# Performance work log

Measured on AMD Instinct MI355X. Metric: run time of the kernel, lower is better.

## Reference

```python
import jax, jax.numpy as jnp
import numpy as np
from jax import lax

B, T, IN, H, NC = 512, 512, 128, 256, 10
GRID_SIZE, SPLINE_ORDER = 5, 3


def _grid(in_f):
    h = 2.0 / GRID_SIZE
    pts = jnp.arange(-SPLINE_ORDER, GRID_SIZE + SPLINE_ORDER + 1, dtype=jnp.float32) * h - 1.0
    return jnp.broadcast_to(pts, (in_f, pts.shape[0]))


def _b_splines(x, grid):
    # x: (B, in); grid: (in, GRID_SIZE + 2*SPLINE_ORDER + 1)
    xg = x[..., None]
    b = ((xg >= grid[:, :-1]) & (xg < grid[:, 1:])).astype(x.dtype)
    for k in range(1, SPLINE_ORDER + 1):
        b = ((xg - grid[:, :-(k + 1)]) / (grid[:, k:-1] - grid[:, :-(k + 1)]) * b[..., :-1]
             + (grid[:, k + 1:] - xg) / (grid[:, k + 1:] - grid[:, 1:-k]) * b[..., 1:])
    return b  # (B, in, GRID_SIZE + SPLINE_ORDER)


def _kan_linear(x, base_w, spline_w, scaler):
    g = _grid(x.shape[-1])
    base = jax.nn.silu(x) @ base_w.T
    spline = jnp.einsum('bik,oik->bo', _b_splines(x, g), spline_w * scaler[..., None])
    return base + spline


def _gru_cell(x, h, wih, whh, bih, bhh):
    gi = x @ wih.T + bih
    gh = h @ whh.T + bhh
    ir, iz, inn = jnp.split(gi, 3, axis=-1)
    hr, hz, hn = jnp.split(gh, 3, axis=-1)
    r = jax.nn.sigmoid(ir + hr)
    z = jax.nn.sigmoid(iz + hz)
    n = jnp.tanh(inn + r * hn)
    return (1.0 - z) * n + z * h


def _lstm_single(x, wih, whh, bih, bhh):
    # single-timestep LSTM with zero initial (h, c); gate order i,f,g,o
    h0 = jnp.zeros((x.shape[0], whh.shape[1]), x.dtype)
    g = x @ wih.T + h0 @ whh.T + bih + bhh
    i, f, gg, o = jnp.split(g, 4, axis=-1)
    c = jax.nn.sigmoid(i) * jnp.tanh(gg)
    return jax.nn.sigmoid(o) * jnp.tanh(c)


def setup_inputs() -> dict:
    keys = iter(jax.random.split(jax.random.key(0), 64))
    def w(*shape):
        return jax.random.normal(next(keys), shape, jnp.float32) * 0.1
    d = {}
    d['x'] = jax.random.normal(next(keys), (B, T, IN), jnp.float32)
    d['gru0_wih'] = w(3 * H, IN); d['gru0_whh'] = w(3 * H, H)
    d['gru0_bih'] = w(3 * H); d['gru0_bhh'] = w(3 * H)
    d['gru1_wih'] = w(3 * H, H); d['gru1_whh'] = w(3 * H, H)
    d['gru1_bih'] = w(3 * H); d['gru1_bhh'] = w(3 * H)
    for suf in ['0', '0r', '1', '1r']:
        d['lw_ih' + suf] = w(512, 256); d['lw_hh' + suf] = w(512, 128)
        d['lb_ih' + suf] = w(512); d['lb_hh' + suf] = w(512)
    d['kan1_base'] = w(64, 256); d['kan1_spline'] = w(64, 256, GRID_SIZE + SPLINE_ORDER); d['kan1_scaler'] = w(64, 256)
    d['kan2_base'] = w(NC, 64); d['kan2_spline'] = w(NC, 64, GRID_SIZE + SPLINE_ORDER); d['kan2_scaler'] = w(NC, 64)
    return d


def reference(x, gru0_wih, gru0_whh, gru0_bih, gru0_bhh, gru1_wih, gru1_whh, gru1_bih, gru1_bhh,
              lw_ih0, lw_hh0, lb_ih0, lb_hh0, lw_ih0r, lw_hh0r, lb_ih0r, lb_hh0r,
              lw_ih1, lw_hh1, lb_ih1, lb_hh1, lw_ih1r, lw_hh1r, lb_ih1r, lb_hh1r,
              kan1_base, kan1_spline, kan1_scaler, kan2_base, kan2_spline, kan2_scaler):
    bsz = x.shape[0]
    h_init = (jnp.zeros((bsz, H), x.dtype), jnp.zeros((bsz, H), x.dtype))

    def step(carry, xt):
        h0, h1 = carry
        h0 = _gru_cell(xt, h0, gru0_wih, gru0_whh, gru0_bih, gru0_bhh)
        h1 = _gru_cell(h0, h1, gru1_wih, gru1_whh, gru1_bih, gru1_bhh)
        return (h0, h1), None

    (h0, h1), _ = lax.scan(step, h_init, jnp.swapaxes(x, 0, 1))  # time-major scan
    s = h1  # last layer final hidden, seq_len-1 single step for LSTM
    o0 = jnp.concatenate([_lstm_single(s, lw_ih0, lw_hh0, lb_ih0, lb_hh0),
                          _lstm_single(s, lw_ih0r, lw_hh0r, lb_ih0r, lb_hh0r)], axis=-1)
    o1 = jnp.concatenate([_lstm_single(o0, lw_ih1, lw_hh1, lb_ih1, lb_hh1),
                          _lstm_single(o0, lw_ih1r, lw_hh1r, lb_ih1r, lb_hh1r)], axis=-1)
    z = _kan_linear(o1, kan1_base, kan1_spline, kan1_scaler)
    return _kan_linear(z, kan2_base, kan2_spline, kan2_scaler)
```

## Files before the change

kernel.cpp:

```cpp
#include <hip/hip_runtime.h>
#include <stdint.h>


constexpr int B_  = 512;
constexpr int T_  = 512;
constexpr int IN_ = 128;
constexpr int H_  = 256;
constexpr int GR_ = 32;
constexpr int PL_ = GR_ * 2 * 4096;
constexpr int TCp = 64;
constexpr int NCp = 8;

typedef __attribute__((ext_vector_type(8))) short bf16x8;
typedef __attribute__((ext_vector_type(4))) float f32x4;

#define MFMA16(a, b, c) __builtin_amdgcn_mfma_f32_16x16x32_bf16((a), (b), (c), 0, 0, 0)

__device__ __forceinline__ float bf2f(unsigned short u){
    union { unsigned int i; float f; } v; v.i = ((unsigned int)u) << 16; return v.f;
}
__device__ __forceinline__ unsigned short f2bf(float f){
    union { float f; unsigned int i; } v; v.f = f;
    return (unsigned short)((v.i + 0x7FFFu + ((v.i >> 16) & 1u)) >> 16);
}
__device__ __forceinline__ unsigned int cvtpk(float a, float b){
    unsigned int r;
    asm("v_cvt_pk_bf16_f32 %0, %1, %2" : "=v"(r) : "v"(a), "v"(b));
    return r;
}
__device__ __forceinline__ unsigned long long pk4(float a, float b, float c, float d){
    const unsigned int lo = cvtpk(a, b), hi = cvtpk(c, d);
    return (unsigned long long)lo | ((unsigned long long)hi << 32);
}
__device__ __forceinline__ float sig_(float x){
    return __builtin_amdgcn_rcpf(1.0f + __expf(-x));
}
__device__ __forceinline__ float tanh_(float x){
    return 1.0f - 2.0f * __builtin_amdgcn_rcpf(1.0f + __expf(2.0f * x));
}
__device__ __forceinline__ bf16x8 ldb8g(const unsigned short* p){ return *(const bf16x8*)p; }

union U64x2 { unsigned long long q[2]; bf16x8 v; };

__device__ __forceinline__ void gl2lds16(const void* g, void* l){
    __builtin_amdgcn_global_load_lds(
        (const __attribute__((address_space(1))) unsigned int*)g,
        (__attribute__((address_space(3))) unsigned int*)l, 16, 0, 0);
}

__global__ void srt_detect(const unsigned int* __restrict__ xw, unsigned int* __restrict__ flag){
    int cnt = 0;
    for (int i = threadIdx.x; i < 1024; i += 64){
        const unsigned int lo = xw[i] & 0xFFFFu;
        const int e = (int)((lo >> 7) & 0xFFu);
        if (e >= 100 && e <= 140) cnt++;
    }
    #pragma unroll
    for (int o = 32; o > 0; o >>= 1) cnt += __shfl_down(cnt, o);
    if (threadIdx.x == 0) *flag = (cnt > 614) ? 1u : 0u;
}

struct ConvTab { const void* src[26]; int n[26]; int off[26]; };

__global__ __launch_bounds__(256) void srt_conv(ConvTab ct, unsigned short* __restrict__ wb,
                                                const unsigned int* __restrict__ flag){
    const bool isb = (*flag != 0);
    const int gsz = gridDim.x * blockDim.x;
    const int gid = blockIdx.x * blockDim.x + threadIdx.x;
    for (int j = 0; j < 26; ++j){
        const int n = ct.n[j];
        unsigned short* o = wb + ct.off[j];
        if (isb){
            const unsigned short* s = (const unsigned short*)ct.src[j];
            for (int i = gid; i < n; i += gsz) o[i] = s[i];
        } else {
            const float* s = (const float*)ct.src[j];
            for (int i = gid; i < n; i += gsz) o[i] = f2bf(s[i]);
        }
    }
}

__global__ __launch_bounds__(256) void srt_prep(
    float* __restrict__ h0s, float* __restrict__ h1s,
    float* __restrict__ bias0, float* __restrict__ bias1,
    const unsigned short* __restrict__ b0ih, const unsigned short* __restrict__ b0hh,
    const unsigned short* __restrict__ b1ih, const unsigned short* __restrict__ b1hh,
    unsigned int* __restrict__ seq)
{
    const int gid = blockIdx.x * blockDim.x + threadIdx.x;
    h0s[gid] = 0.f;
    h1s[gid] = 0.f;
    if (gid < 768){
        bias0[gid] = bf2f(b0ih[gid]) + (gid < 512 ? bf2f(b0hh[gid]) : 0.f);
        bias1[gid] = bf2f(b1ih[gid]) + (gid < 512 ? bf2f(b1hh[gid]) : 0.f);
    }
    if (gid < 1024) seq[gid] = 0u;
}

__device__ void seq_dev(unsigned short* shm,
    const unsigned short* __restrict__ gi,
    const unsigned short* __restrict__ whh,
    const unsigned short* __restrict__ bhh,
    float* __restrict__ hstate,
    unsigned short* __restrict__ h_all,
    const int TC, const int bg)
{
    unsigned short* wnL   = shm;
    unsigned short* hbufB = shm + 32768;
    unsigned short* gibB  = shm + 32768 + 8192;

    const int tid  = threadIdx.x;
    const int lane = tid & 63;
    const int wv   = tid >> 6;
    const int l15  = lane & 15;
    const int quad = lane >> 4;
    const int m0   = bg * 16;
    const int swz  = (l15 & 7) << 4;

    bf16x8 wr[5][8];
    #pragma unroll
    for (int fi = 0; fi < 6; ++fi){
        const int u = fi >> 1, ii = fi & 1;
        const unsigned short* wp =
            whh + (size_t)(u * 256 + wv * 32 + ii * 16 + l15) * 256 + quad * 8;
        if (fi < 5){
            #pragma unroll
            for (int kc = 0; kc < 8; ++kc) wr[fi][kc] = ldb8g(wp + kc * 32);
        } else {
            #pragma unroll
            for (int kc = 0; kc < 8; ++kc)
                *(bf16x8*)&wnL[((wv * 8 + kc) << 9) + lane * 8] = ldb8g(wp + kc * 32);
        }
    }

    f32x4 bn0[2];
    #pragma unroll
    for (int ii = 0; ii < 2; ++ii)
        #pragma unroll
        for (int j = 0; j < 4; ++j)
            bn0[ii][j] = bf2f(bhh[512 + wv * 32 + ii * 16 + quad * 4 + j]);

    f32x4 hr[2];
    #pragma unroll
    for (int ii = 0; ii < 2; ++ii)
        hr[ii] = *(const f32x4*)&hstate[(size_t)(m0 + l15) * 256 + wv * 32 + ii * 16 + quad * 4];

    const unsigned short* gpp[3]; int gdl[3];
    #pragma unroll
    for (int i = 0; i < 3; ++i){
        const int g_  = i * 512 + tid;
        const int row = g_ / 96;
        const int cg  = g_ - row * 96;
        gpp[i] = gi + ((size_t)m0 + row) * 768 + ((cg ^ (row & 7)) << 3);
        gdl[i] = g_ * 8;
    }

    #pragma unroll
    for (int ii = 0; ii < 2; ++ii){
        const unsigned long long pk = pk4(hr[ii][0], hr[ii][1], hr[ii][2], hr[ii][3]);
        *(unsigned long long*)((char*)hbufB + l15 * 512 +
            ((wv * 64 + ii * 32 + quad * 8) ^ swz)) = pk;
    }
    #pragma unroll
    for (int i = 0; i < 3; ++i) gl2lds16(gpp[i], &gibB[gdl[i]]);
    __syncthreads();

    #pragma unroll 1
    for (int t = 0; t < TC; ++t){
        const int par = t & 1;
        unsigned short* hb_cur = hbufB + par * 4096;
        unsigned short* hb_nxt = hbufB + (par ^ 1) * 4096;
        unsigned short* gb_cur = gibB + par * 12288;
        unsigned short* gb_nxt = gibB + (par ^ 1) * 12288;

        if (t + 1 < TC){
            const size_t toff = (size_t)(t + 1) * (512 * 768);
            #pragma unroll
            for (int i = 0; i < 3; ++i) gl2lds16(gpp[i] + toff, &gb_nxt[gdl[i]]);
        }

        f32x4 aR0 = {0,0,0,0}, aR1 = {0,0,0,0}, aZ0 = {0,0,0,0}, aZ1 = {0,0,0,0};
        f32x4 aN0 = bn0[0], aN1 = bn0[1];
        __builtin_amdgcn_s_setprio(1);
        #pragma unroll
        for (int kc = 0; kc < 8; ++kc){
            const bf16x8 hb = *(const bf16x8*)((const char*)hb_cur +
                l15 * 512 + ((kc * 64 + quad * 16) ^ swz));
            const bf16x8 w5 = *(const bf16x8*)&wnL[((wv * 8 + kc) << 9) + lane * 8];
            aR0 = MFMA16(wr[0][kc], hb, aR0);
            aR1 = MFMA16(wr[1][kc], hb, aR1);
            aZ0 = MFMA16(wr[2][kc], hb, aZ0);
            aZ1 = MFMA16(wr[3][kc], hb, aZ1);
            aN0 = MFMA16(wr[4][kc], hb, aN0);
            aN1 = MFMA16(w5,        hb, aN1);
        }
        __builtin_amdgcn_s_setprio(0);

        const char* gbase = (const char*)gb_cur + l15 * 1536;
        #pragma unroll
        for (int ii = 0; ii < 2; ++ii){
            const int cb = wv * 64 + ii * 32 + quad * 8;
            const unsigned long long qr = *(const unsigned long long*)(gbase + ((       cb) ^ swz));
            const unsigned long long qz = *(const unsigned long long*)(gbase + ((512  + cb) ^ swz));
            const unsigned long long qn = *(const unsigned long long*)(gbase + ((1024 + cb) ^ swz));
            const f32x4 aR = ii ? aR1 : aR0;
            const f32x4 aZ = ii ? aZ1 : aZ0;
            const f32x4 aN = ii ? aN1 : aN0;
            #pragma unroll
            for (int j = 0; j < 4; ++j){
                const float rr = sig_(aR[j] + bf2f((unsigned short)(qr >> (16 * j))));
                const float zz = sig_(aZ[j] + bf2f((unsigned short)(qz >> (16 * j))));
                const float nn = tanh_(bf2f((unsigned short)(qn >> (16 * j))) + rr * aN[j]);
                hr[ii][j] = (1.0f - zz) * nn + zz * hr[ii][j];
            }
        }

        #pragma unroll
        for (int ii = 0; ii < 2; ++ii){
            const unsigned long long pk = pk4(hr[ii][0], hr[ii][1], hr[ii][2], hr[ii][3]);
            *(unsigned long long*)((char*)hb_nxt + l15 * 512 +
                ((wv * 64 + ii * 32 + quad * 8) ^ swz)) = pk;
            if (h_all)
                *(unsigned long long*)(h_all + ((size_t)t * 512 + m0 + l15) * 256 +
                    wv * 32 + ii * 16 + quad * 4) = pk;
        }

        __syncthreads();
    }

    #pragma unroll
    for (int ii = 0; ii < 2; ++ii)
        *(f32x4*)&hstate[(size_t)(m0 + l15) * 256 + wv * 32 + ii * 16 + quad * 4] = hr[ii];
}

template<int K, bool XS>
__device__ void gemm_dev(unsigned short* shm, const void* Asrc, const bool isb,
                         const int t0, const unsigned short* __restrict__ W,
                         const float* __restrict__ bias,
                         unsigned short* __restrict__ C, const int mb)
{
    unsigned short* Ares = shm;

    const int tid = threadIdx.x;
    const int lane = tid & 63, wv = tid >> 6;
    const int l15 = lane & 15, quad = lane >> 4;
    const int rh = wv & 1, fq = wv >> 1;

    constexpr int GPT = K / 32;
    constexpr int GPR = K / 8;
    constexpr int NK  = K / 64;
    constexpr int NIT = 6 * NK;

    if (!XS || isb){
        #pragma unroll
        for (int i = 0; i < GPT; ++i){
            const int g_ = i * 512 + tid;
            const int row = g_ / GPR, cg = g_ % GPR;
            size_t src;
            if (XS){
                const int r = mb * 128 + row;
                const int b = r & 511, tt = r >> 9;
                src = ((size_t)b * 512 + (t0 + tt)) * 128 + ((cg ^ (row & 7)) << 3);
            } else {
                src = (size_t)(mb * 128 + row) * K + ((cg ^ (row & 7)) << 3);
            }
            gl2lds16((const unsigned short*)Asrc + src, &Ares[g_ * 8]);
        }
    } else {
        #pragma unroll
        for (int i = 0; i < GPT; ++i){
            const int g_ = i * 512 + tid;
            const int row = g_ / GPR, cg = g_ % GPR;
            const int r = mb * 128 + row;
            const int b = r & 511, tt = r >> 9;
            const float* p = (const float*)Asrc + ((size_t)b * 512 + (t0 + tt)) * 128 + cg * 8;
            const float4 f0 = *(const float4*)p;
            const float4 f1 = *(const float4*)(p + 4);
            uint4 u;
            u.x = cvtpk(f0.x, f0.y); u.y = cvtpk(f0.z, f0.w);
            u.z = cvtpk(f1.x, f1.y); u.w = cvtpk(f1.z, f1.w);
            *(uint4*)&Ares[(row * GPR + (cg ^ (row & 7))) * 8] = u;
        }
    }

    auto stageW = [&](int i){
        const int Nb = i / NK, k0 = (i % NK) * 64;
        unsigned short* dst = shm + 32768 + (i % 3) * 8192;
        #pragma unroll
        for (int j = 0; j < 2; ++j){
            const int g_ = j * 512 + tid;
            const int row = g_ >> 3, cg = g_ & 7;
            gl2lds16(W + (size_t)(Nb * 128 + row) * K + k0 + ((cg ^ (row & 7)) << 3),
                     &dst[g_ * 8]);
        }
    };

    stageW(0);
    stageW(1);
    if (XS && !isb) asm volatile("s_waitcnt lgkmcnt(0)" ::: "memory");

    for (int Nb = 0; Nb < 6; ++Nb){
        f32x4 acc[4][2];
        #pragma unroll
        for (int mi = 0; mi < 4; ++mi){
            acc[mi][0] = (f32x4){0,0,0,0};
            acc[mi][1] = (f32x4){0,0,0,0};
        }

        #pragma unroll
        for (int kk = 0; kk < NK; ++kk){
            const int i = Nb * NK + kk;
            if (Nb == 0 && kk == 0)      asm volatile("s_waitcnt vmcnt(2)"  ::: "memory");
            else if (kk == 0)            asm volatile("s_waitcnt vmcnt(10)" ::: "memory");
            else                         asm volatile("s_waitcnt vmcnt(2)"  ::: "memory");
            __builtin_amdgcn_s_barrier();
            __builtin_amdgcn_sched_barrier(0);
            if (i + 2 < NIT) stageW(i + 2);

            const unsigned short* wbuf = shm + 32768 + (i % 3) * 8192;
            #pragma unroll
            for (int kc = 0; kc < 2; ++kc){
                bf16x8 wf[2], af[4];
                #pragma unroll
                for (int ni = 0; ni < 2; ++ni){
                    const int rf = fq * 32 + ni * 16 + l15;
                    wf[ni] = *(const bf16x8*)((const char*)wbuf +
                        rf * 128 + (((kc * 4 + quad) ^ (rf & 7)) << 4));
                }
                #pragma unroll
                for (int mi = 0; mi < 4; ++mi){
                    const int ra = rh * 64 + mi * 16 + l15;
                    af[mi] = *(const bf16x8*)((const char*)Ares +
                        ra * (2 * K) + (((kk * 8 + kc * 4 + quad) ^ (ra & 7)) << 4));
                }
                #pragma unroll
                for (int mi = 0; mi < 4; ++mi){
                    acc[mi][0] = MFMA16(wf[0], af[mi], acc[mi][0]);
                    acc[mi][1] = MFMA16(wf[1], af[mi], acc[mi][1]);
                }
            }
        }

        float bs[2][4];
        #pragma unroll
        for (int ni = 0; ni < 2; ++ni)
            #pragma unroll
            for (int j = 0; j < 4; ++j)
                bs[ni][j] = bias[Nb * 128 + fq * 32 + ni * 16 + quad * 4 + j];
        #pragma unroll
        for (int mi = 0; mi < 4; ++mi)
            #pragma unroll
            for (int ni = 0; ni < 2; ++ni){
                const unsigned int lo = cvtpk(acc[mi][ni][0] + bs[ni][0],
                                              acc[mi][ni][1] + bs[ni][1]);
                const unsigned int hi = cvtpk(acc[mi][ni][2] + bs[ni][2],
                                              acc[mi][ni][3] + bs[ni][3]);
                const int row = mb * 128 + rh * 64 + mi * 16 + l15;
                const int col = Nb * 128 + fq * 32 + ni * 16 + quad * 4;
                uint2 st; st.x = lo; st.y = hi;
                *(uint2*)(C + (size_t)row * 768 + col) = st;
            }
    }
}

struct PA {
    const void* xv;
    const unsigned int* flag;
    const unsigned short *w0ih, *w0hh, *b0hh, *w1ih, *w1hh, *b1hh;
    const float *bias0, *bias1;
    float *h0s, *h1s;
    unsigned short *gi0a, *gi0b, *haa, *hab, *gi1a, *gi1b;
    int p;
};

__global__ __launch_bounds__(512, 1) void srt_phase(PA a){
    __shared__ __align__(16) unsigned short shm[65536];
    const int bid = blockIdx.x;
    const int p = a.p;

    if (bid < 32){
        const int c = p - 1; if (c < 0 || c >= NCp) return;
        seq_dev(shm, (c & 1) ? a.gi0b : a.gi0a, a.w0hh, a.b0hh, a.h0s,
                (c & 1) ? a.hab : a.haa, TCp, bid);
    } else if (bid < 64){
        const int c = p - 3; if (c < 0 || c >= NCp) return;
        seq_dev(shm, (c & 1) ? a.gi1b : a.gi1a, a.w1hh, a.b1hh, a.h1s,
                nullptr, TCp, bid - 32);
    } else if (bid < 320){
        const int c = p; if (c >= NCp) return;
        const bool isb = (*a.flag != 0);
        gemm_dev<128, true>(shm, a.xv, isb, c * TCp, a.w0ih, a.bias0,
                            (c & 1) ? a.gi0b : a.gi0a, bid - 64);
    } else {
        const int c = p - 2; if (c < 0 || c >= NCp) return;
        gemm_dev<256, false>(shm, (c & 1) ? a.hab : a.haa, true, 0, a.w1ih, a.bias1,
                             (c & 1) ? a.gi1b : a.gi1a, bid - 320);
    }
}

__global__ __launch_bounds__(256, 1) void srt_gru(
    const void* __restrict__ xv,
    const unsigned short* __restrict__ w0ih,
    const unsigned short* __restrict__ w0hh,
    const unsigned short* __restrict__ b0ih,
    const unsigned short* __restrict__ b0hh,
    const unsigned short* __restrict__ w1ih,
    const unsigned short* __restrict__ w1hh,
    const unsigned short* __restrict__ b1ih,
    const unsigned short* __restrict__ b1hh,
    float* __restrict__ s_out,
    const unsigned int* __restrict__ flagp,
    unsigned int* __restrict__ seq,
    unsigned short* __restrict__ hb)
{
    __shared__ __align__(16) unsigned short w0hhL[4 * 24 * 512];

    const bool isb = (*flagp != 0);
    const int tid  = threadIdx.x;
    const int lane = tid & 63;
    const int wv   = tid >> 6;
    const int l15  = lane & 15;
    const int quad = lane >> 4;
    const int q    = blockIdx.x >> 5;
    const int g    = blockIdx.x & 31;
    const int m0   = g * 16;
    const int c    = q * 64 + wv * 16 + l15;

    bf16x8 w0ihr[3][4];
    #pragma unroll
    for (int u = 0; u < 3; ++u)
        #pragma unroll
        for (int kc = 0; kc < 4; ++kc)
            w0ihr[u][kc] = ldb8g(w0ih + (u * 256 + c) * IN_ + kc * 32 + quad * 8);

    bf16x8 w1ihr[3][8], w1hhr[3][8];
    #pragma unroll
    for (int u = 0; u < 3; ++u)
        #pragma unroll
        for (int kc = 0; kc < 8; ++kc){
            w1ihr[u][kc] = ldb8g(w1ih + (u * 256 + c) * H_ + kc * 32 + quad * 8);
            w1hhr[u][kc] = ldb8g(w1hh + (u * 256 + c) * H_ + kc * 32 + quad * 8);
        }

    const int wl = wv * 12288 + lane * 8;
    #pragma unroll
    for (int u = 0; u < 3; ++u)
        #pragma unroll
        for (int kc = 0; kc < 8; ++kc){
            const bf16x8 f = ldb8g(w0hh + (u * 256 + c) * H_ + kc * 32 + quad * 8);
            *(bf16x8*)&w0hhL[wl + (u * 8 + kc) * 512] = f;
        }

    const float brz0a = bf2f(b0ih[c])       + bf2f(b0hh[c]);
    const float brz0b = bf2f(b0ih[256 + c]) + bf2f(b0hh[256 + c]);
    const float bni0v = bf2f(b0ih[512 + c]);
    const float bnh0v = bf2f(b0hh[512 + c]);
    const float brz1a = bf2f(b1ih[c])       + bf2f(b1hh[c]);
    const float brz1b = bf2f(b1ih[256 + c]) + bf2f(b1hh[256 + c]);
    const float bni1v = bf2f(b1ih[512 + c]);
    const float bnh1v = bf2f(b1hh[512 + c]);
    __syncthreads();

    float h0r[4] = {0.f, 0.f, 0.f, 0.f};
    float h1r[4] = {0.f, 0.f, 0.f, 0.f};

    const size_t xrow = (size_t)(m0 + l15) * (T_ * IN_) + quad * 8;
    const unsigned short* pxb = (const unsigned short*)xv + xrow;
    const float*          pxf = (const float*)xv + xrow;

    unsigned int* sq = seq + g * 32;
    const int wr_row[4] = {(quad * 4 + 0) * 256 + c, (quad * 4 + 1) * 256 + c,
                           (quad * 4 + 2) * 256 + c, (quad * 4 + 3) * 256 + c};

    const f32x4 z4 = {0.f, 0.f, 0.f, 0.f};
    bf16x8 h0A[8], h1A[8];
    #pragma unroll
    for (int kc = 0; kc < 8; ++kc){
        h0A[kc] = (bf16x8)(short)0;
        h1A[kc] = (bf16x8)(short)0;
    }

    #pragma unroll 1
    for (int t = 0; t < T_; ++t){
        const int par = t & 1;
        const unsigned int tgt = 4u * (unsigned)(t + 1);
        unsigned short* plane = hb + par * PL_ + g * (2 * 4096);

        #pragma unroll
        for (int j = 0; j < 4; ++j)
            __hip_atomic_store(&plane[4096 + wr_row[j]], f2bf(h1r[j]),
                               __ATOMIC_RELAXED, __HIP_MEMORY_SCOPE_AGENT);

        bf16x8 ax[4];
        if (isb){
            #pragma unroll
            for (int kc = 0; kc < 4; ++kc) ax[kc] = ldb8g(pxb + t * IN_ + kc * 32);
        } else {
            #pragma unroll
            for (int kc = 0; kc < 4; ++kc){
                const float* p = pxf + t * IN_ + kc * 32;
                const float4 f0 = *(const float4*)p;
                const float4 f1 = *(const float4*)(p + 4);
                bf16x8 a;
                a[0] = (short)f2bf(f0.x); a[1] = (short)f2bf(f0.y);
                a[2] = (short)f2bf(f0.z); a[3] = (short)f2bf(f0.w);
                a[4] = (short)f2bf(f1.x); a[5] = (short)f2bf(f1.y);
                a[6] = (short)f2bf(f1.z); a[7] = (short)f2bf(f1.w);
                ax[kc] = a;
            }
        }

        f32x4 Tr = z4, Tz = z4, Tni = z4, Tnh = z4;
        #pragma unroll
        for (int kc = 0; kc < 4; ++kc){
            Tr  = MFMA16(ax[kc], w0ihr[0][kc], Tr);
            Tz  = MFMA16(ax[kc], w0ihr[1][kc], Tz);
            Tni = MFMA16(ax[kc], w0ihr[2][kc], Tni);
        }
        #pragma unroll
        for (int kc = 0; kc < 8; ++kc){
            const bf16x8 a = h0A[kc];
            Tr  = MFMA16(a, *(const bf16x8*)&w0hhL[wl + (0 * 8 + kc) * 512], Tr);
            Tz  = MFMA16(a, *(const bf16x8*)&w0hhL[wl + (1 * 8 + kc) * 512], Tz);
            Tnh = MFMA16(a, *(const bf16x8*)&w0hhL[wl + (2 * 8 + kc) * 512], Tnh);
        }
        #pragma unroll
        for (int j = 0; j < 4; ++j){
            const float rr = sig_(Tr[j] + brz0a);
            const float zz = sig_(Tz[j] + brz0b);
            const float nn = tanh_(Tni[j] + bni0v + rr * (Tnh[j] + bnh0v));
            h0r[j] = (1.0f - zz) * nn + zz * h0r[j];
        }

        #pragma unroll
        for (int j = 0; j < 4; ++j)
            __hip_atomic_store(&plane[wr_row[j]], f2bf(h0r[j]),
                               __ATOMIC_RELAXED, __HIP_MEMORY_SCOPE_AGENT);

        __syncthreads();
        if (tid == 0)
            __hip_atomic_fetch_add(sq, 1u, __ATOMIC_RELAXED, __HIP_MEMORY_SCOPE_AGENT);
        if (lane == 0){
            while (__hip_atomic_load(sq, __ATOMIC_RELAXED, __HIP_MEMORY_SCOPE_AGENT) < tgt)
                __builtin_amdgcn_s_sleep(1);
        }
        __atomic_signal_fence(__ATOMIC_ACQ_REL);

        {
            const unsigned short* r0 = plane + l15 * 256 + quad * 8;
            #pragma unroll
            for (int kc = 0; kc < 8; ++kc){
                U64x2 u0, u1;
                u0.q[0] = __hip_atomic_load((const unsigned long long*)(r0 + kc * 32),
                                            __ATOMIC_RELAXED, __HIP_MEMORY_SCOPE_AGENT);
                u0.q[1] = __hip_atomic_load((const unsigned long long*)(r0 + kc * 32 + 4),
                                            __ATOMIC_RELAXED, __HIP_MEMORY_SCOPE_AGENT);
                u1.q[0] = __hip_atomic_load((const unsigned long long*)(r0 + 4096 + kc * 32),
                                            __ATOMIC_RELAXED, __HIP_MEMORY_SCOPE_AGENT);
                u1.q[1] = __hip_atomic_load((const unsigned long long*)(r0 + 4096 + kc * 32 + 4),
                                            __ATOMIC_RELAXED, __HIP_MEMORY_SCOPE_AGENT);
                h0A[kc] = u0.v;
                h1A[kc] = u1.v;
            }
        }

        Tr = z4; Tz = z4; Tni = z4; Tnh = z4;
        #pragma unroll
        for (int kc = 0; kc < 8; ++kc){
            const bf16x8 a0 = h0A[kc];
            const bf16x8 a1 = h1A[kc];
            Tr  = MFMA16(a0, w1ihr[0][kc], Tr);
            Tr  = MFMA16(a1, w1hhr[0][kc], Tr);
            Tz  = MFMA16(a0, w1ihr[1][kc], Tz);
            Tz  = MFMA16(a1, w1hhr[1][kc], Tz);
            Tni = MFMA16(a0, w1ihr[2][kc], Tni);
            Tnh = MFMA16(a1, w1hhr[2][kc], Tnh);
        }
        #pragma unroll
        for (int j = 0; j < 4; ++j){
            const float rr = sig_(Tr[j] + brz1a);
            const float zz = sig_(Tz[j] + brz1b);
            const float nn = tanh_(Tni[j] + bni1v + rr * (Tnh[j] + bnh1v));
            h1r[j] = (1.0f - zz) * nn + zz * h1r[j];
        }
    }

    #pragma unroll
    for (int j = 0; j < 4; ++j)
        s_out[(size_t)(m0 + quad * 4 + j) * H_ + c] = h1r[j];
}

__device__ __forceinline__ float knot_(int p){ return (float)(p - 3) * 0.4f - 1.0f; }

__device__ __forceinline__ void bspline8(float xv, float* bb8){
    float bb[11];
    #pragma unroll
    for (int p = 0; p < 11; ++p)
        bb[p] = (xv >= knot_(p) && xv < knot_(p + 1)) ? 1.f : 0.f;
    #pragma unroll
    for (int k = 1; k <= 3; ++k){
        #pragma unroll
        for (int p = 0; p <= 10 - k; ++p){
            const float tp = knot_(p), tpk = knot_(p + k);
            const float tp1 = knot_(p + 1), tpk1 = knot_(p + k + 1);
            bb[p] = (xv - tp) / (tpk - tp) * bb[p] + (tpk1 - xv) / (tpk1 - tp1) * bb[p + 1];
        }
    }
    #pragma unroll
    for (int j = 0; j < 8; ++j) bb8[j] = bb[j];
}

__device__ __forceinline__ void lstm_part(const float* sxv, const unsigned short* w,
                                          int uu, int k0, float* out3){
    const unsigned short* wi = w + (size_t)uu * 256 + k0;
    const unsigned short* wg = w + (size_t)(256 + uu) * 256 + k0;
    const unsigned short* wo = w + (size_t)(384 + uu) * 256 + k0;
    float ai = 0.f, ag = 0.f, ao = 0.f;
    for (int k = 0; k < 64; k += 8){
        const bf16x8 vi = ldb8g(wi + k);
        const bf16x8 vg = ldb8g(wg + k);
        const bf16x8 vo = ldb8g(wo + k);
        #pragma unroll
        for (int j = 0; j < 8; ++j){
            const float s = sxv[k0 + k + j];
            ai += bf2f((unsigned short)vi[j]) * s;
            ag += bf2f((unsigned short)vg[j]) * s;
            ao += bf2f((unsigned short)vo[j]) * s;
        }
    }
    out3[0] = ai; out3[1] = ag; out3[2] = ao;
}

__global__ __launch_bounds__(1024) void srt_tail(
    const float* __restrict__ in,
    const unsigned short* __restrict__ w0f, const unsigned short* __restrict__ bi0f,
    const unsigned short* __restrict__ bh0f,
    const unsigned short* __restrict__ w0r, const unsigned short* __restrict__ bi0r,
    const unsigned short* __restrict__ bh0r,
    const unsigned short* __restrict__ w1f, const unsigned short* __restrict__ bi1f,
    const unsigned short* __restrict__ bh1f,
    const unsigned short* __restrict__ w1r, const unsigned short* __restrict__ bi1r,
    const unsigned short* __restrict__ bh1r,
    const unsigned short* __restrict__ k1b, const unsigned short* __restrict__ k1s,
    const unsigned short* __restrict__ k1c,
    const unsigned short* __restrict__ k2b, const unsigned short* __restrict__ k2s,
    const unsigned short* __restrict__ k2c,
    void* __restrict__ outp,
    const unsigned int* __restrict__ flagp)
{
    __shared__ float sx[256];
    __shared__ float sy[256];
    __shared__ float part[4][256][3];
    __shared__ float sil[256];
    __shared__ float spl[256][8];
    __shared__ float red16[64][16];
    __shared__ float sil2[64];
    __shared__ float spl2[64][8];
    __shared__ float red2[10][16];

    const int b = blockIdx.x, tid = threadIdx.x;
    const int qr = tid >> 8, sub = tid & 255;
    const int dir = sub >> 7, uu = sub & 127;

    if (tid < 256) sx[tid] = in[b * 256 + tid];
    __syncthreads();

    float p3[3];
    lstm_part(sx, dir ? w0r : w0f, uu, qr * 64, p3);
    part[qr][sub][0] = p3[0]; part[qr][sub][1] = p3[1]; part[qr][sub][2] = p3[2];
    __syncthreads();
    if (tid < 256){
        const unsigned short* bi = dir ? bi0r : bi0f;
        const unsigned short* bh = dir ? bh0r : bh0f;
        const float ai = part[0][sub][0] + part[1][sub][0] + part[2][sub][0] + part[3][sub][0];
        const float ag = part[0][sub][1] + part[1][sub][1] + part[2][sub][1] + part[3][sub][1];
        const float ao = part[0][sub][2] + part[1][sub][2] + part[2][sub][2] + part[3][sub][2];
        const float gi = ai + bf2f(bi[uu])       + bf2f(bh[uu]);
        const float gg = ag + bf2f(bi[256 + uu]) + bf2f(bh[256 + uu]);
        const float go = ao + bf2f(bi[384 + uu]) + bf2f(bh[384 + uu]);
        sy[sub] = sig_(go) * tanh_(sig_(gi) * tanh_(gg));
    }
    __syncthreads();

    lstm_part(sy, dir ? w1r : w1f, uu, qr * 64, p3);
    part[qr][sub][0] = p3[0]; part[qr][sub][1] = p3[1]; part[qr][sub][2] = p3[2];
    __syncthreads();
    if (tid < 256){
        const unsigned short* bi = dir ? bi1r : bi1f;
        const unsigned short* bh = dir ? bh1r : bh1f;
        const float ai = part[0][sub][0] + part[1][sub][0] + part[2][sub][0] + part[3][sub][0];
        const float ag = part[0][sub][1] + part[1][sub][1] + part[2][sub][1] + part[3][sub][1];
        const float ao = part[0][sub][2] + part[1][sub][2] + part[2][sub][2] + part[3][sub][2];
        const float gi = ai + bf2f(bi[uu])       + bf2f(bh[uu]);
        const float gg = ag + bf2f(bi[256 + uu]) + bf2f(bh[256 + uu]);
        const float go = ao + bf2f(bi[384 + uu]) + bf2f(bh[384 + uu]);
        const float o1v = sig_(go) * tanh_(sig_(gi) * tanh_(gg));
        sil[sub] = o1v * sig_(o1v);
        float bb[8];
        bspline8(o1v, bb);
        #pragma unroll
        for (int j = 0; j < 8; ++j) spl[sub][j] = bb[j];
    }
    __syncthreads();

    {
        const int o = tid >> 4, q16 = tid & 15;
        float acc = 0.f;
        for (int k = q16 * 16; k < q16 * 16 + 16; ++k){
            acc += sil[k] * bf2f(k1b[o * 256 + k]);
            float t = 0.f;
            #pragma unroll
            for (int j = 0; j < 8; ++j) t += spl[k][j] * bf2f(k1s[(o * 256 + k) * 8 + j]);
            acc += t * bf2f(k1c[o * 256 + k]);
        }
        red16[o][q16] = acc;
    }
    __syncthreads();
    if (tid < 64){
        float zv = 0.f;
        #pragma unroll
        for (int i = 0; i < 16; ++i) zv += red16[tid][i];
        sil2[tid] = zv * sig_(zv);
        float b2[8];
        bspline8(zv, b2);
        #pragma unroll
        for (int j = 0; j < 8; ++j) spl2[tid][j] = b2[j];
    }
    __syncthreads();

    if (tid < 160){
        const int o2 = tid >> 4, q = tid & 15;
        float a2 = 0.f;
        for (int k = q * 4; k < q * 4 + 4; ++k){
            a2 += sil2[k] * bf2f(k2b[o2 * 64 + k]);
            float t = 0.f;
            #pragma unroll
            for (int j = 0; j < 8; ++j) t += spl2[k][j] * bf2f(k2s[(o2 * 64 + k) * 8 + j]);
            a2 += t * bf2f(k2c[o2 * 64 + k]);
        }
        red2[o2][q] = a2;
    }
    __syncthreads();
    if (tid < 10){
        float a2 = 0.f;
        #pragma unroll
        for (int i = 0; i < 16; ++i) a2 += red2[tid][i];
        if (*flagp) ((unsigned short*)outp)[b * 10 + tid] = f2bf(a2);
        else        ((float*)outp)[b * 10 + tid] = a2;
    }
}

extern "C" void kernel_launch(void* const* d_in, const int* in_sizes, int n_in,
                              void* d_out, int out_size, void* d_ws, size_t ws_size,
                              hipStream_t stream)
{
    unsigned int* flag = (unsigned int*)d_ws;
    float* s = (float*)((char*)d_ws + 16);
    unsigned short* wb = (unsigned short*)(s + 512 * 256);

    const int idxs[26] = {1,2,3,4,5,6,7,8, 9,11,12, 13,15,16, 17,19,20, 21,23,24,
                          25,26,27, 28,29,30};
    ConvTab ct;
    int off = 0;
    int offs[26];
    for (int j = 0; j < 26; ++j){
        ct.src[j] = d_in[idxs[j]];
        ct.n[j]   = in_sizes[idxs[j]];
        ct.off[j] = off;
        offs[j]   = off;
        off += in_sizes[idxs[j]];
    }
    uintptr_t p = (uintptr_t)(wb + off);
    p = (p + 255) & ~(uintptr_t)255;
    unsigned int* seq = (unsigned int*)p;
    unsigned short* hb = (unsigned short*)(seq + 1024);
    p = (uintptr_t)(hb + 2 * 32 * 2 * 4096);
    p = (p + 255) & ~(uintptr_t)255;
    float* h0s   = (float*)p;
    float* bias0 = h0s + 512 * 256;
    float* bias1 = bias0 + 768;
    p = (uintptr_t)(bias1 + 768);
    p = (p + 255) & ~(uintptr_t)255;
    char* dyn = (char*)p;
    const size_t used = (size_t)(dyn - (char*)d_ws);

    const size_t slab_gi = (size_t)TCp * 512 * 768;
    const size_t slab_ha = (size_t)TCp * 512 * 256;
    const size_t pipe_need = used + (4 * slab_gi + 2 * slab_ha) * sizeof(unsigned short);
    const bool pipe_ok = pipe_need <= ws_size;

    const unsigned short *w0ih = wb + offs[0],  *w0hh = wb + offs[1];
    const unsigned short *b0ih = wb + offs[2],  *b0hh = wb + offs[3];
    const unsigned short *w1ih = wb + offs[4],  *w1hh = wb + offs[5];
    const unsigned short *b1ih = wb + offs[6],  *b1hh = wb + offs[7];
    const unsigned short *lwih0  = wb + offs[8],  *lbih0  = wb + offs[9],  *lbhh0  = wb + offs[10];
    const unsigned short *lwih0r = wb + offs[11], *lbih0r = wb + offs[12], *lbhh0r = wb + offs[13];
    const unsigned short *lwih1  = wb + offs[14], *lbih1  = wb + offs[15], *lbhh1  = wb + offs[16];
    const unsigned short *lwih1r = wb + offs[17], *lbih1r = wb + offs[18], *lbhh1r = wb + offs[19];
    const unsigned short *k1b = wb + offs[20], *k1s = wb + offs[21], *k1c = wb + offs[22];
    const unsigned short *k2b = wb + offs[23], *k2s = wb + offs[24], *k2c = wb + offs[25];

    srt_detect<<<1, 64, 0, stream>>>((const unsigned int*)d_in[0], flag);
    srt_conv<<<1024, 256, 0, stream>>>(ct, wb, flag);
    srt_prep<<<512, 256, 0, stream>>>(h0s, s, bias0, bias1, b0ih, b0hh, b1ih, b1hh, seq);

    if (pipe_ok){
        unsigned short* gi0a = (unsigned short*)dyn;
        unsigned short* gi0b = gi0a + slab_gi;
        unsigned short* haa  = gi0b + slab_gi;
        unsigned short* hab  = haa + slab_ha;
        unsigned short* gi1a = hab + slab_ha;
        unsigned short* gi1b = gi1a + slab_gi;

        PA a;
        a.xv = d_in[0]; a.flag = flag;
        a.w0ih = w0ih; a.w0hh = w0hh; a.b0hh = b0hh;
        a.w1ih = w1ih; a.w1hh = w1hh; a.b1hh = b1hh;
        a.bias0 = bias0; a.bias1 = bias1;
        a.h0s = h0s; a.h1s = s;
        a.gi0a = gi0a; a.gi0b = gi0b; a.haa = haa; a.hab = hab;
        a.gi1a = gi1a; a.gi1b = gi1b;
        for (int ph = 0; ph <= NCp + 2; ++ph){
            a.p = ph;
            srt_phase<<<576, 512, 0, stream>>>(a);
        }
    } else {
        srt_gru<<<128, 256, 0, stream>>>(d_in[0], w0ih, w0hh, b0ih, b0hh,
                                         w1ih, w1hh, b1ih, b1hh, s, flag, seq, hb);
    }

    srt_tail<<<512, 1024, 0, stream>>>(s,
        lwih0, lbih0, lbhh0, lwih0r, lbih0r, lbhh0r,
        lwih1, lbih1, lbhh1, lwih1r, lbih1r, lbhh1r,
        k1b, k1s, k1c, k2b, k2s, k2c, d_out, flag);
}
```

Before: 1.752 ms.

## Restructure input-projection GEMMs to keep weight slice resident and stream activations

The input-projection GEMMs inside the phased kernel are rewritten. Each block now loads a 64-column weight slice once into LDS and holds its fragments in registers, then streams 32 double-buffered 128-row activation tiles, instead of holding a 128-row activation tile and streaming all weight tiles. The grid shrinks from 576 to 256 blocks (96 per GEMM). This aims to cut redundant weight traffic and block count, but gives less parallelism per phase, smaller per-wave MFMA tiles and a full barrier per k-step.

```diff
diff --git a/kernel.cpp b/kernel.cpp
--- a/kernel.cpp
+++ b/kernel.cpp
@@ -237,126 +237,121 @@
 __device__ void gemm_dev(unsigned short* shm, const void* Asrc, const bool isb,
                          const int t0, const unsigned short* __restrict__ W,
                          const float* __restrict__ bias,
-                         unsigned short* __restrict__ C, const int mb)
+                         unsigned short* __restrict__ C,
+                         const int nb, const int mg)
 {
-    unsigned short* Ares = shm;
+    unsigned short* Wt = shm;
+    unsigned short* Ab = shm + 64 * K;
 
     const int tid = threadIdx.x;
     const int lane = tid & 63, wv = tid >> 6;
     const int l15 = lane & 15, quad = lane >> 4;
-    const int rh = wv & 1, fq = wv >> 1;
-
-    constexpr int GPT = K / 32;
-    constexpr int GPR = K / 8;
+    const int fh = wv & 1, mq = wv >> 1;
     constexpr int NK  = K / 64;
-    constexpr int NIT = 6 * NK;
-
-    if (!XS || isb){
-        #pragma unroll
-        for (int i = 0; i < GPT; ++i){
+    constexpr int GW  = K / 8;
+    constexpr int WG  = 64 * GW / 512;
+    constexpr int NIT = 32 * NK;
+
+    #pragma unroll
+    for (int i = 0; i < WG; ++i){
+        const int g_ = i * 512 + tid;
+        const int row = g_ / GW, cg = g_ % GW;
+        gl2lds16(W + (size_t)(nb * 64 + row) * K + ((cg ^ (row & 7)) << 3), &Wt[g_ * 8]);
+    }
+
+    float bs[2][4];
+    #pragma unroll
+    for (int ni = 0; ni < 2; ++ni)
+        #pragma unroll
+        for (int j = 0; j < 4; ++j)
+            bs[ni][j] = bias[nb * 64 + fh * 32 + ni * 16 + quad * 4 + j];
+
+    auto stageA = [&](int it){
+        const int mt = it / NK, kk = it % NK;
+        unsigned short* dst = Ab + (it & 1) * 8192;
+        #pragma unroll
+        for (int i = 0; i < 2; ++i){
             const int g_ = i * 512 + tid;
-            const int row = g_ / GPR, cg = g_ % GPR;
-            size_t src;
+            const int row = g_ >> 3, cg = g_ & 7;
+            const int r = mg * 4096 + mt * 128 + row;
             if (XS){
-                const int r = mb * 128 + row;
                 const int b = r & 511, tt = r >> 9;
-                src = ((size_t)b * 512 + (t0 + tt)) * 128 + ((cg ^ (row & 7)) << 3);
+                const size_t s0 = ((size_t)b * 512 + (t0 + tt)) * 128 + kk * 64;
+                if (isb){
+                    gl2lds16((const unsigned short*)Asrc + s0 + ((cg ^ (row & 7)) << 3),
+                             &dst[g_ * 8]);
+                } else {
+                    const float* p = (const float*)Asrc + s0 + cg * 8;
+                    const float4 f0 = *(const float4*)p;
+                    const float4 f1 = *(const float4*)(p + 4);
+                    uint4 u;
+                    u.x = cvtpk(f0.x, f0.y); u.y = cvtpk(f0.z, f0.w);
+                    u.z = cvtpk(f1.x, f1.y); u.w = cvtpk(f1.z, f1.w);
+                    *(uint4*)&dst[(row * 8 + (cg ^ (row & 7))) * 8] = u;
+                }
             } else {
-                src = (size_t)(mb * 128 + row) * K + ((cg ^ (row & 7)) << 3);
+                gl2lds16((const unsigned short*)Asrc + (size_t)r * K + kk * 64 +
+                         ((cg ^ (row & 7)) << 3), &dst[g_ * 8]);
             }
-            gl2lds16((const unsigned short*)Asrc + src, &Ares[g_ * 8]);
-        }
-    } else {
-        #pragma unroll
-        for (int i = 0; i < GPT; ++i){
-            const int g_ = i * 512 + tid;
-            const int row = g_ / GPR, cg = g_ % GPR;
-            const int r = mb * 128 + row;
-            const int b = r & 511, tt = r >> 9;
-            const float* p = (const float*)Asrc + ((size_t)b * 512 + (t0 + tt)) * 128 + cg * 8;
-            const float4 f0 = *(const float4*)p;
-            const float4 f1 = *(const float4*)(p + 4);
-            uint4 u;
-            u.x = cvtpk(f0.x, f0.y); u.y = cvtpk(f0.z, f0.w);
-            u.z = cvtpk(f1.x, f1.y); u.w = cvtpk(f1.z, f1.w);
-            *(uint4*)&Ares[(row * GPR + (cg ^ (row & 7))) * 8] = u;
-        }
-    }
-
-    auto stageW = [&](int i){
-        const int Nb = i / NK, k0 = (i % NK) * 64;
-        unsigned short* dst = shm + 32768 + (i % 3) * 8192;
-        #pragma unroll
-        for (int j = 0; j < 2; ++j){
-            const int g_ = j * 512 + tid;
-            const int row = g_ >> 3, cg = g_ & 7;
-            gl2lds16(W + (size_t)(Nb * 128 + row) * K + k0 + ((cg ^ (row & 7)) << 3),
-                     &dst[g_ * 8]);
         }
     };
 
-    stageW(0);
-    stageW(1);
-    if (XS && !isb) asm volatile("s_waitcnt lgkmcnt(0)" ::: "memory");
-
-    for (int Nb = 0; Nb < 6; ++Nb){
-        f32x4 acc[4][2];
-        #pragma unroll
-        for (int mi = 0; mi < 4; ++mi){
-            acc[mi][0] = (f32x4){0,0,0,0};
-            acc[mi][1] = (f32x4){0,0,0,0};
+    stageA(0);
+    __syncthreads();
+
+    bf16x8 wf[2][2 * NK];
+    #pragma unroll
+    for (int ni = 0; ni < 2; ++ni)
+        #pragma unroll
+        for (int k2 = 0; k2 < 2 * NK; ++k2){
+            const int rf = fh * 32 + ni * 16 + l15;
+            wf[ni][k2] = *(const bf16x8*)((const char*)Wt +
+                rf * (2 * K) + (((k2 * 4 + quad) ^ (rf & 7)) << 4));
+        }
+
+    #pragma unroll 1
+    for (int mt = 0; mt < 32; ++mt){
+        f32x4 acc[2][2];
+        #pragma unroll
+        for (int ni = 0; ni < 2; ++ni){
+            acc[ni][0] = (f32x4){0,0,0,0};
+            acc[ni][1] = (f32x4){0,0,0,0};
         }
 
         #pragma unroll
         for (int kk = 0; kk < NK; ++kk){
-            const int i = Nb * NK + kk;
-            if (Nb == 0 && kk == 0)      asm volatile("s_waitcnt vmcnt(2)"  ::: "memory");
-            else if (kk == 0)            asm volatile("s_waitcnt vmcnt(10)" ::: "memory");
-            else                         asm volatile("s_waitcnt vmcnt(2)"  ::: "memory");
-            __builtin_amdgcn_s_barrier();
-            __builtin_amdgcn_sched_barrier(0);
-            if (i + 2 < NIT) stageW(i + 2);
-
-            const unsigned short* wbuf = shm + 32768 + (i % 3) * 8192;
+            const int it = mt * NK + kk;
+            if (it) __syncthreads();
+            if (it + 1 < NIT) stageA(it + 1);
+
+            const char* ab = (const char*)(Ab + (it & 1) * 8192);
             #pragma unroll
             for (int kc = 0; kc < 2; ++kc){
-                bf16x8 wf[2], af[4];
+                bf16x8 af[2];
                 #pragma unroll
-                for (int ni = 0; ni < 2; ++ni){
-                    const int rf = fq * 32 + ni * 16 + l15;
-                    wf[ni] = *(const bf16x8*)((const char*)wbuf +
-                        rf * 128 + (((kc * 4 + quad) ^ (rf & 7)) << 4));
+                for (int mi = 0; mi < 2; ++mi){
+                    const int ra = mq * 32 + mi * 16 + l15;
+                    af[mi] = *(const bf16x8*)(ab + ra * 128 +
+                              (((kc * 4 + quad) ^ (ra & 7)) << 4));
                 }
                 #pragma unroll
-                for (int mi = 0; mi < 4; ++mi){
-                    const int ra = rh * 64 + mi * 16 + l15;
-                    af[mi] = *(const bf16x8*)((const char*)Ares +
-                        ra * (2 * K) + (((kk * 8 + kc * 4 + quad) ^ (ra & 7)) << 4));
-                }
-                #pragma unroll
-                for (int mi = 0; mi < 4; ++mi){
-                    acc[mi][0] = MFMA16(wf[0], af[mi], acc[mi][0]);
-                    acc[mi][1] = MFMA16(wf[1], af[mi], acc[mi][1]);
-                }
+                for (int ni = 0; ni < 2; ++ni)
+                    #pragma unroll
+                    for (int mi = 0; mi < 2; ++mi)
+                        acc[ni][mi] = MFMA16(wf[ni][kk * 2 + kc], af[mi], acc[ni][mi]);
             }
         }
 
-        float bs[2][4];
         #pragma unroll
         for (int ni = 0; ni < 2; ++ni)
             #pragma unroll
-            for (int j = 0; j < 4; ++j)
-                bs[ni][j] = bias[Nb * 128 + fq * 32 + ni * 16 + quad * 4 + j];
-        #pragma unroll
-        for (int mi = 0; mi < 4; ++mi)
-            #pragma unroll
-            for (int ni = 0; ni < 2; ++ni){
-                const unsigned int lo = cvtpk(acc[mi][ni][0] + bs[ni][0],
-                                              acc[mi][ni][1] + bs[ni][1]);
-                const unsigned int hi = cvtpk(acc[mi][ni][2] + bs[ni][2],
-                                              acc[mi][ni][3] + bs[ni][3]);
-                const int row = mb * 128 + rh * 64 + mi * 16 + l15;
-                const int col = Nb * 128 + fq * 32 + ni * 16 + quad * 4;
+            for (int mi = 0; mi < 2; ++mi){
+                const unsigned int lo = cvtpk(acc[ni][mi][0] + bs[ni][0],
+                                              acc[ni][mi][1] + bs[ni][1]);
+                const unsigned int hi = cvtpk(acc[ni][mi][2] + bs[ni][2],
+                                              acc[ni][mi][3] + bs[ni][3]);
+                const int row = mg * 4096 + mt * 128 + mq * 32 + mi * 16 + l15;
+                const int col = nb * 64 + fh * 32 + ni * 16 + quad * 4;
                 uint2 st; st.x = lo; st.y = hi;
                 *(uint2*)(C + (size_t)row * 768 + col) = st;
             }
@@ -386,15 +381,17 @@
         const int c = p - 3; if (c < 0 || c >= NCp) return;
         seq_dev(shm, (c & 1) ? a.gi1b : a.gi1a, a.w1hh, a.b1hh, a.h1s,
                 nullptr, TCp, bid - 32);
-    } else if (bid < 320){
+    } else if (bid < 160){
         const int c = p; if (c >= NCp) return;
         const bool isb = (*a.flag != 0);
+        const int idx = bid - 64;
         gemm_dev<128, true>(shm, a.xv, isb, c * TCp, a.w0ih, a.bias0,
-                            (c & 1) ? a.gi0b : a.gi0a, bid - 64);
+                            (c & 1) ? a.gi0b : a.gi0a, idx % 12, idx / 12);
     } else {
         const int c = p - 2; if (c < 0 || c >= NCp) return;
+        const int idx = bid - 160;
         gemm_dev<256, false>(shm, (c & 1) ? a.hab : a.haa, true, 0, a.w1ih, a.bias1,
-                             (c & 1) ? a.gi1b : a.gi1a, bid - 320);
+                             (c & 1) ? a.gi1b : a.gi1a, idx % 12, idx / 12);
     }
 }
 
@@ -822,7 +819,7 @@
         a.gi1a = gi1a; a.gi1b = gi1b;
         for (int ph = 0; ph <= NCp + 2; ++ph){
             a.p = ph;
-            srt_phase<<<576, 512, 0, stream>>>(a);
+            srt_phase<<<256, 512, 0, stream>>>(a);
         }
     } else {
         srt_gru<<<128, 256, 0, stream>>>(d_in[0], w0ih, w0hh, b0ih, b0hh,
```

Result: slower. 1.851 ms (+5.7%).
